# Kernel tuning notes

Hardware: AMD Instinct MI355X
Metric: run time of the kernel (lower is better)

## Reference

```python
import jax, jax.numpy as jnp
import numpy as np

GROUPS = 32
EPS = 1e-5
NUM_HEADS = 8

def group_norm(x, w, b):
    # x: [B, C, H, W], normalize over (C//G, H, W) per group
    B, C, H, W = x.shape
    xg = x.reshape(B, GROUPS, C // GROUPS, H, W)
    mean = xg.mean(axis=(2, 3, 4), keepdims=True)
    var = xg.var(axis=(2, 3, 4), keepdims=True)
    xg = (xg - mean) * jax.lax.rsqrt(var + EPS)
    x = xg.reshape(B, C, H, W)
    return x * w[None, :, None, None] + b[None, :, None, None]

def setup_inputs() -> dict:
    key = jax.random.key(0)
    ks = jax.random.split(key, 3)
    C = 512
    x = jax.random.normal(ks[0], (8, C, 32, 32), dtype=jnp.float32)
    gn_w = jnp.ones((C,), jnp.float32)
    gn_b = jnp.zeros((C,), jnp.float32)
    # 1x1 conv weights stored as [out, in] matrices
    qkv_w = jax.random.normal(ks[1], (3 * C, C), dtype=jnp.float32) * (C ** -0.5)
    qkv_b = jnp.zeros((3 * C,), jnp.float32)
    proj_w = jax.random.normal(ks[2], (C, C), dtype=jnp.float32) * (C ** -0.5)
    proj_b = jnp.zeros((C,), jnp.float32)
    return {"x": x, "gn_w": gn_w, "gn_b": gn_b, "qkv_w": qkv_w,
            "qkv_b": qkv_b, "proj_w": proj_w, "proj_b": proj_b}

def reference(x, gn_w, gn_b, qkv_w, qkv_b, proj_w, proj_b):
    B, C, H, W = x.shape
    nh = NUM_HEADS
    hd = C // nh
    N = H * W
    residual = x
    xn = group_norm(x, gn_w, gn_b)
    # 1x1 conv == channel matmul: [B, 3C, H, W]
    qkv = jnp.einsum('bchw,oc->bohw', xn, qkv_w) + qkv_b[None, :, None, None]
    # [B, 3, nh, hd, N] -> q/k/v each [B, nh, N, hd]
    qkv = qkv.reshape(B, 3, nh, hd, N).transpose(1, 0, 2, 4, 3)
    q, k, v = qkv[0], qkv[1], qkv[2]
    scale = hd ** -0.5
    attn = jnp.einsum('bhqd,bhkd->bhqk', q, k) * scale
    attn = jax.nn.softmax(attn, axis=-1)
    out = jnp.einsum('bhqk,bhkd->bhqd', attn, v)  # [B, nh, N, hd]
    out = out.transpose(0, 1, 3, 2).reshape(B, C, H, W)
    out = jnp.einsum('bchw,oc->bohw', out, proj_w) + proj_b[None, :, None, None]
    return out + residual
```

## Files before the change

kernel.cpp:

```cpp
#include <hip/hip_runtime.h>


typedef __bf16 bf16;
typedef __bf16 bf16x8 __attribute__((ext_vector_type(8)));
typedef __bf16 bf16x4 __attribute__((ext_vector_type(4)));
typedef float  f32x4  __attribute__((ext_vector_type(4)));
typedef float  f32x16 __attribute__((ext_vector_type(16)));
typedef unsigned u32x4 __attribute__((ext_vector_type(4)));

#define MFMA_16x16x32(A, B, C) __builtin_amdgcn_mfma_f32_16x16x32_bf16((A), (B), (C), 0, 0, 0)
#define MFMA_32x32x16(A, B, C) __builtin_amdgcn_mfma_f32_32x32x16_bf16((A), (B), (C), 0, 0, 0)

static __device__ __forceinline__ unsigned cvt_pk_bf16(float a, float b) {
  unsigned r;
  asm("v_cvt_pk_bf16_f32 %0, %1, %2" : "=v"(r) : "v"(a), "v"(b));
  return r;
}

static __device__ __forceinline__ void async_stage_128x32(
    const bf16* __restrict__ g0, bf16* lds, int tid) {
  const int wv = tid >> 6, ln = tid & 63;
#pragma unroll
  for (int cc = 0; cc < 2; ++cc) {
    const int c = wv + cc * 4;
    const bf16* g = g0 + (size_t)(c * 16 + (ln >> 2)) * 512 + (ln & 3) * 8;
    __builtin_amdgcn_global_load_lds(
        (const __attribute__((address_space(1))) void*)g,
        (__attribute__((address_space(3))) void*)(lds + c * 512),
        16, 0, 0);
  }
}

static __device__ __forceinline__ void async_stage_64x32(
    const bf16* __restrict__ g0, bf16* lds, int tid) {
  const int wv = tid >> 6, ln = tid & 63;
  const bf16* g = g0 + (size_t)(wv * 16 + (ln >> 2)) * 512 + (ln & 3) * 8;
  __builtin_amdgcn_global_load_lds(
      (const __attribute__((address_space(1))) void*)g,
      (__attribute__((address_space(3))) void*)(lds + wv * 512),
      16, 0, 0);
}

__global__ __launch_bounds__(256) void gn_fused_kernel(
    const float* __restrict__ x,
    const float* __restrict__ gn_w, const float* __restrict__ gn_b,
    const float* __restrict__ qw, const float* __restrict__ pw,
    bf16* __restrict__ wq, bf16* __restrict__ wp, bf16* __restrict__ xn_t) {
  const int t = threadIdx.x;
  if (blockIdx.x >= 256) {
    const int idx = (blockIdx.x - 256) * 256 + t;
    if (idx < 196608) {
      float4 v = ((const float4*)qw)[idx];
      bf16x4 o = { (bf16)v.x, (bf16)v.y, (bf16)v.z, (bf16)v.w };
      *(bf16x4*)(&wq[idx * 4]) = o;
    }
    if (idx < 65536) {
      float4 v = ((const float4*)pw)[idx];
      bf16x4 o = { (bf16)v.x, (bf16)v.y, (bf16)v.z, (bf16)v.w };
      *(bf16x4*)(&wp[idx * 4]) = o;
    }
    return;
  }
  const int bg = blockIdx.x;
  const int b = bg >> 5, g = bg & 31;
  const int c0 = g * 16;
  const float4* p = (const float4*)(x + ((size_t)b * 512 + c0) * 1024);
  float4 v[16];
  float s = 0.f, s2 = 0.f;
#pragma unroll
  for (int i = 0; i < 16; ++i) {
    v[i] = p[t + 256 * i];
    s  += (v[i].x + v[i].y) + (v[i].z + v[i].w);
    s2 += (v[i].x * v[i].x + v[i].y * v[i].y) + (v[i].z * v[i].z + v[i].w * v[i].w);
  }
#pragma unroll
  for (int d = 1; d < 64; d <<= 1) {
    s  += __shfl_xor(s,  d);
    s2 += __shfl_xor(s2, d);
  }
  __shared__ float as[4], as2[4];
  __shared__ float scs[16], shs[16];
  if ((t & 63) == 0) { as[t >> 6] = s; as2[t >> 6] = s2; }
  __syncthreads();
  if (t < 16) {
    float S  = as[0] + as[1] + as[2] + as[3];
    float S2 = as2[0] + as2[1] + as2[2] + as2[3];
    float m  = S * (1.0f / 16384.0f);
    float rs = rsqrtf(S2 * (1.0f / 16384.0f) - m * m + 1e-5f);
    float sc = rs * gn_w[c0 + t];
    scs[t] = sc;
    shs[t] = gn_b[c0 + t] - m * sc;
  }
  __syncthreads();
  bf16* ob = xn_t + ((size_t)b * 1024 + 4 * t) * 512 + c0;
#pragma unroll
  for (int j = 0; j < 4; ++j) {
    bf16 tmp[16];
#pragma unroll
    for (int i = 0; i < 16; ++i) {
      float val = (j == 0) ? v[i].x : (j == 1) ? v[i].y : (j == 2) ? v[i].z : v[i].w;
      tmp[i] = (bf16)(val * scs[i] + shs[i]);
    }
    *(bf16x8*)(ob + (size_t)j * 512)     = *(bf16x8*)(tmp);
    *(bf16x8*)(ob + (size_t)j * 512 + 8) = *(bf16x8*)(tmp + 8);
  }
}

__global__ __launch_bounds__(256) void qkv_gemm_kernel(
    const bf16* __restrict__ W, const bf16* __restrict__ xn_t,
    const float* __restrict__ qkv_b, bf16* __restrict__ qkv_t,
    bf16* __restrict__ v_t) {
  const int n0 = blockIdx.x * 128;
  const int o0 = blockIdx.y * 128;
  const int b  = blockIdx.z;
  __shared__ bf16 As[2][128 * 32];
  __shared__ bf16 Bs[2][128 * 32];
  const int tid = threadIdx.x, ln = tid & 63, wv = tid >> 6;
  const int mw = (wv >> 1) * 64, nw = (wv & 1) * 64;
  const int l15 = ln & 15, lg = ln >> 4;
  const bool isV = (o0 >= 1024);
  const bf16* gA = W + (size_t)o0 * 512;
  const bf16* gB = xn_t + ((size_t)b * 1024 + n0) * 512;
  f32x4 acc[4][4] = {};
  async_stage_128x32(gA, As[0], tid);
  async_stage_128x32(gB, Bs[0], tid);
  for (int it = 0; it < 16; ++it) {
    __syncthreads();
    const int cur = it & 1, nxt = cur ^ 1;
    if (it < 15) {
      async_stage_128x32(gA + (it + 1) * 32, As[nxt], tid);
      async_stage_128x32(gB + (it + 1) * 32, Bs[nxt], tid);
    }
    bf16x8 af[4], bfr[4];
#pragma unroll
    for (int mi = 0; mi < 4; ++mi)
      af[mi] = *(const bf16x8*)(&As[cur][(mw + mi * 16 + l15) * 32 + lg * 8]);
#pragma unroll
    for (int nj = 0; nj < 4; ++nj)
      bfr[nj] = *(const bf16x8*)(&Bs[cur][(nw + nj * 16 + l15) * 32 + lg * 8]);
    if (!isV) {
#pragma unroll
      for (int mi = 0; mi < 4; ++mi)
#pragma unroll
        for (int nj = 0; nj < 4; ++nj)
          acc[mi][nj] = MFMA_16x16x32(af[mi], bfr[nj], acc[mi][nj]);
    } else {
#pragma unroll
      for (int mi = 0; mi < 4; ++mi)
#pragma unroll
        for (int nj = 0; nj < 4; ++nj)
          acc[mi][nj] = MFMA_16x16x32(bfr[nj], af[mi], acc[mi][nj]);
    }
  }
  if (!isV) {
    const float qs = (o0 < 512) ? 0.125f * 1.44269504089f : 1.0f;
#pragma unroll
    for (int mi = 0; mi < 4; ++mi) {
      const int o = o0 + mw + mi * 16 + lg * 4;
      const float b0 = qkv_b[o], b1 = qkv_b[o + 1], b2 = qkv_b[o + 2], b3 = qkv_b[o + 3];
#pragma unroll
      for (int nj = 0; nj < 4; ++nj) {
        const int n = n0 + nw + nj * 16 + l15;
        f32x4 v = acc[mi][nj];
        bf16x4 st = { (bf16)((v.x + b0) * qs), (bf16)((v.y + b1) * qs),
                      (bf16)((v.z + b2) * qs), (bf16)((v.w + b3) * qs) };
        *(bf16x4*)(&qkv_t[((size_t)b * 1024 + n) * 1536 + o]) = st;
      }
    }
  } else {
#pragma unroll
    for (int mi = 0; mi < 4; ++mi) {
      const int o  = o0 + mw + mi * 16 + l15;
      const int hd = o - 1024;
      const float bias = qkv_b[o];
#pragma unroll
      for (int nj = 0; nj < 4; ++nj) {
        const int n = n0 + nw + nj * 16 + lg * 4;
        f32x4 v = acc[mi][nj];
        bf16x4 st = { (bf16)(v.x + bias), (bf16)(v.y + bias),
                      (bf16)(v.z + bias), (bf16)(v.w + bias) };
        *(bf16x4*)(&v_t[((size_t)b * 512 + hd) * 1024 + n]) = st;
      }
    }
  }
}

__global__ __launch_bounds__(512, 4) void attn_kernel(
    const bf16* __restrict__ qkv_t, const bf16* __restrict__ v_t,
    bf16* __restrict__ at_t) {
  const int qt = blockIdx.y;
  const int b  = blockIdx.x >> 3;
  const int h  = blockIdx.x & 7;
  __shared__ __align__(16) char smem[73728];
  const int tid = threadIdx.x, ln = tid & 63, wv = tid >> 6;
  const int half = wv >> 2, w4 = wv & 3;
  const int l31 = ln & 31, hi = ln >> 5;
  const bf16* hq  = qkv_t + (size_t)b * 1024 * 1536 + h * 64;
  const bf16* hk  = hq + 512;
  const bf16* vtb = v_t + (size_t)(b * 8 + h) * 64 * 1024;

  const int qb = qt * 128 + w4 * 32;
  bf16x8 qf[4];
#pragma unroll
  for (int ks = 0; ks < 4; ++ks)
    qf[ks] = *(const bf16x8*)(hq + (size_t)(qb + l31) * 1536 + ks * 16 + hi * 8);

  f32x16 oacc[2] = {};
  float lst = 0.f;

  const int t256 = tid & 255;
  const int srow = t256 >> 2, scg = (t256 & 3) * 16;
  const int kt0 = half * 8;

  bf16x8 k0r, k1r, v0r, v1r;
  {
    const bf16* gk = hk  + (size_t)(kt0 * 64 + srow) * 1536 + scg;
    const bf16* gv = vtb + (size_t)srow * 1024 + kt0 * 64 + scg;
    k0r = *(const bf16x8*)(gk);
    k1r = *(const bf16x8*)(gk + 8);
    v0r = *(const bf16x8*)(gv);
    v1r = *(const bf16x8*)(gv + 8);
    bf16* Kt = (bf16*)(smem + half * 18432);
    bf16* Vt = Kt + 64 * 72;
    *(bf16x8*)(&Kt[srow * 72 + scg])     = k0r;
    *(bf16x8*)(&Kt[srow * 72 + scg + 8]) = k1r;
    *(bf16x8*)(&Vt[srow * 72 + scg])     = v0r;
    *(bf16x8*)(&Vt[srow * 72 + scg + 8]) = v1r;
  }

  for (int i = 0; i < 8; ++i) {
    __syncthreads();
    if (i < 7) {
      const int kt = kt0 + i + 1;
      const bf16* gk = hk  + (size_t)(kt * 64 + srow) * 1536 + scg;
      const bf16* gv = vtb + (size_t)srow * 1024 + kt * 64 + scg;
      k0r = *(const bf16x8*)(gk);
      k1r = *(const bf16x8*)(gk + 8);
      v0r = *(const bf16x8*)(gv);
      v1r = *(const bf16x8*)(gv + 8);
    }
    const bf16* Kt = (const bf16*)(smem + (i & 1) * 36864 + half * 18432);
    const bf16* Vt = Kt + 64 * 72;

#pragma unroll
    for (int kk = 0; kk < 2; ++kk) {
      const int kvb = kk * 32;
      f32x16 st = {};
      __builtin_amdgcn_s_setprio(1);
#pragma unroll
      for (int ks = 0; ks < 4; ++ks) {
        bf16x8 kf = *(const bf16x8*)(&Kt[(kvb + l31) * 72 + ks * 16 + hi * 8]);
        st = MFMA_32x32x16(kf, qf[ks], st);
      }
      __builtin_amdgcn_s_setprio(0);
#pragma unroll
      for (int r = 0; r < 16; ++r) st[r] = exp2f(st[r]);
      lst += ((st[0] + st[1]) + (st[2] + st[3])) + ((st[4] + st[5]) + (st[6] + st[7]))
           + ((st[8] + st[9]) + (st[10] + st[11])) + ((st[12] + st[13]) + (st[14] + st[15]));
#pragma unroll
      for (int t = 0; t < 2; ++t) {
        unsigned x0 = cvt_pk_bf16(st[t * 8 + 0], st[t * 8 + 1]);
        unsigned x1 = cvt_pk_bf16(st[t * 8 + 2], st[t * 8 + 3]);
        unsigned y0 = cvt_pk_bf16(st[t * 8 + 4], st[t * 8 + 5]);
        unsigned y1 = cvt_pk_bf16(st[t * 8 + 6], st[t * 8 + 7]);
        asm("v_permlane32_swap_b32 %0, %1" : "+v"(x0), "+v"(y0));
        asm("v_permlane32_swap_b32 %0, %1" : "+v"(x1), "+v"(y1));
        u32x4 pu = { x0, x1, y0, y1 };
        bf16x8 pb = __builtin_bit_cast(bf16x8, pu);
        __builtin_amdgcn_s_setprio(1);
#pragma unroll
        for (int dt = 0; dt < 2; ++dt) {
          bf16x8 vf = *(const bf16x8*)(&Vt[(dt * 32 + l31) * 72 + kvb + t * 16 + hi * 8]);
          oacc[dt] = MFMA_32x32x16(vf, pb, oacc[dt]);
        }
        __builtin_amdgcn_s_setprio(0);
      }
    }

    if (i < 7) {
      bf16* Ktn = (bf16*)(smem + ((i + 1) & 1) * 36864 + half * 18432);
      bf16* Vtn = Ktn + 64 * 72;
      *(bf16x8*)(&Ktn[srow * 72 + scg])     = k0r;
      *(bf16x8*)(&Ktn[srow * 72 + scg + 8]) = k1r;
      *(bf16x8*)(&Vtn[srow * 72 + scg])     = v0r;
      *(bf16x8*)(&Vtn[srow * 72 + scg + 8]) = v1r;
    }
  }

  const float lf = lst + __shfl_xor(lst, 32);

  float* MB  = (float*)smem;
  float* MLb = (float*)(smem + 34816);
  __syncthreads();
  if (half == 1) {
    float* mb = MB + w4 * (32 * 68);
#pragma unroll
    for (int dt = 0; dt < 2; ++dt)
#pragma unroll
      for (int rr = 0; rr < 4; ++rr) {
        f32x4 v = { oacc[dt][rr * 4 + 0], oacc[dt][rr * 4 + 1],
                    oacc[dt][rr * 4 + 2], oacc[dt][rr * 4 + 3] };
        *(f32x4*)(mb + l31 * 68 + dt * 32 + rr * 8 + hi * 4) = v;
      }
    if (hi == 0) MLb[w4 * 32 + l31] = lf;
  }
  __syncthreads();
  if (half == 0) {
    const float* mb = MB + w4 * (32 * 68);
    const float inv = 1.0f / (lf + MLb[w4 * 32 + l31]);
    const int q = qb + l31;
    bf16* ob = at_t + ((size_t)b * 1024 + q) * 512 + h * 64;
#pragma unroll
    for (int dt = 0; dt < 2; ++dt)
#pragma unroll
      for (int rr = 0; rr < 4; ++rr) {
        f32x4 obv = *(const f32x4*)(mb + l31 * 68 + dt * 32 + rr * 8 + hi * 4);
        bf16x4 ov = { (bf16)((oacc[dt][rr * 4 + 0] + obv[0]) * inv),
                      (bf16)((oacc[dt][rr * 4 + 1] + obv[1]) * inv),
                      (bf16)((oacc[dt][rr * 4 + 2] + obv[2]) * inv),
                      (bf16)((oacc[dt][rr * 4 + 3] + obv[3]) * inv) };
        *(bf16x4*)(ob + dt * 32 + rr * 8 + hi * 4) = ov;
      }
  }
}

__global__ __launch_bounds__(256) void proj_gemm_kernel(
    const bf16* __restrict__ at_t, const bf16* __restrict__ wp,
    const float* __restrict__ proj_b, const float* __restrict__ x,
    float* __restrict__ out) {
  const int i0 = blockIdx.x * 64;
  const int c0 = blockIdx.y * 128;
  const int b  = blockIdx.z;
  __shared__ bf16 As[2][64 * 32];
  __shared__ bf16 Bs[2][128 * 32];
  const int tid = threadIdx.x, ln = tid & 63, wv = tid >> 6;
  const int mw = (wv >> 1) * 32, nw = (wv & 1) * 64;
  const int l15 = ln & 15, lg = ln >> 4;
  const bf16* gA = at_t + ((size_t)b * 1024 + i0) * 512;
  const bf16* gB = wp + (size_t)c0 * 512;
  f32x4 acc[2][4] = {};
  async_stage_64x32(gA, As[0], tid);
  async_stage_128x32(gB, Bs[0], tid);
  for (int it = 0; it < 16; ++it) {
    __syncthreads();
    const int cur = it & 1, nxt = cur ^ 1;
    if (it < 15) {
      async_stage_64x32(gA + (it + 1) * 32, As[nxt], tid);
      async_stage_128x32(gB + (it + 1) * 32, Bs[nxt], tid);
    }
    bf16x8 af[2], bfr[4];
#pragma unroll
    for (int mi = 0; mi < 2; ++mi)
      af[mi] = *(const bf16x8*)(&As[cur][(mw + mi * 16 + l15) * 32 + lg * 8]);
#pragma unroll
    for (int nj = 0; nj < 4; ++nj)
      bfr[nj] = *(const bf16x8*)(&Bs[cur][(nw + nj * 16 + l15) * 32 + lg * 8]);
#pragma unroll
    for (int mi = 0; mi < 2; ++mi)
#pragma unroll
      for (int nj = 0; nj < 4; ++nj)
        acc[mi][nj] = MFMA_16x16x32(af[mi], bfr[nj], acc[mi][nj]);
  }
#pragma unroll
  for (int mi = 0; mi < 2; ++mi) {
    const int i = i0 + mw + mi * 16 + lg * 4;
#pragma unroll
    for (int nj = 0; nj < 4; ++nj) {
      const int c = c0 + nw + nj * 16 + l15;
      const float bias = proj_b[c];
      const size_t off = ((size_t)b * 512 + c) * 1024 + i;
      const float4 res = *(const float4*)(x + off);
      f32x4 v = acc[mi][nj];
      float4 ov;
      ov.x = v.x + bias + res.x;
      ov.y = v.y + bias + res.y;
      ov.z = v.z + bias + res.z;
      ov.w = v.w + bias + res.w;
      *(float4*)(out + off) = ov;
    }
  }
}

extern "C" void kernel_launch(void* const* d_in, const int* in_sizes, int n_in,
                              void* d_out, int out_size, void* d_ws, size_t ws_size,
                              hipStream_t stream) {
  (void)in_sizes; (void)n_in; (void)out_size; (void)ws_size;
  const float* x      = (const float*)d_in[0];
  const float* gn_w   = (const float*)d_in[1];
  const float* gn_b   = (const float*)d_in[2];
  const float* qkv_w  = (const float*)d_in[3];
  const float* qkv_b  = (const float*)d_in[4];
  const float* proj_w = (const float*)d_in[5];
  const float* proj_b = (const float*)d_in[6];
  float* out = (float*)d_out;

  char* ws = (char*)d_ws;
  bf16* wq    = (bf16*)ws;
  bf16* wp    = wq + (size_t)1536 * 512;
  bf16* xn_t  = wp + (size_t)512 * 512;
  bf16* qkv_t = xn_t + (size_t)8 * 1024 * 512;
  bf16* at_t  = qkv_t + (size_t)8 * 1024 * 1536;
  bf16* v_t   = at_t + (size_t)8 * 1024 * 512;

  hipLaunchKernelGGL(gn_fused_kernel, dim3(1280),     dim3(256), 0, stream,
                     x, gn_w, gn_b, qkv_w, proj_w, wq, wp, xn_t);
  hipLaunchKernelGGL(qkv_gemm_kernel, dim3(8, 12, 8), dim3(256), 0, stream,
                     wq, xn_t, qkv_b, qkv_t, v_t);
  hipLaunchKernelGGL(attn_kernel,     dim3(64, 8),    dim3(512), 0, stream,
                     qkv_t, v_t, at_t);
  hipLaunchKernelGGL(proj_gemm_kernel,dim3(16, 4, 8), dim3(256), 0, stream,
                     at_t, wp, proj_b, x, out);
}
```

Baseline: 156.7 us.

## Stage attention K/V tiles via async global_load_lds with XOR-swizzled LDS

```diff
diff --git a/kernel.cpp b/kernel.cpp
--- a/kernel.cpp
+++ b/kernel.cpp
@@ -185,13 +185,38 @@
   }
 }
 
+static __device__ __forceinline__ void attn_stage(
+    const bf16* __restrict__ hk, const bf16* __restrict__ vtb,
+    char* bufbase, int it, int wv, int ln) {
+  const int hh = wv >> 2;
+  const int kt = hh * 8 + it;
+  const int r8 = ln >> 3;
+  const int e0 = ((ln & 7) ^ r8) * 8;
+  char* base = bufbase + hh * 16384;
+#pragma unroll
+  for (int j = 0; j < 2; ++j) {
+    const int g = (wv & 3) * 2 + j;
+    const int row = g * 8 + r8;
+    const bf16* gk = hk + (size_t)(kt * 64 + row) * 1536 + e0;
+    __builtin_amdgcn_global_load_lds(
+        (const __attribute__((address_space(1))) void*)gk,
+        (__attribute__((address_space(3))) void*)(base + g * 1024),
+        16, 0, 0);
+    const bf16* gv = vtb + (size_t)row * 1024 + kt * 64 + e0;
+    __builtin_amdgcn_global_load_lds(
+        (const __attribute__((address_space(1))) void*)gv,
+        (__attribute__((address_space(3))) void*)(base + 8192 + g * 1024),
+        16, 0, 0);
+  }
+}
+
 __global__ __launch_bounds__(512, 4) void attn_kernel(
     const bf16* __restrict__ qkv_t, const bf16* __restrict__ v_t,
     bf16* __restrict__ at_t) {
   const int qt = blockIdx.y;
   const int b  = blockIdx.x >> 3;
   const int h  = blockIdx.x & 7;
-  __shared__ __align__(16) char smem[73728];
+  __shared__ __align__(16) char smem[65536];
   const int tid = threadIdx.x, ln = tid & 63, wv = tid >> 6;
   const int half = wv >> 2, w4 = wv & 3;
   const int l31 = ln & 31, hi = ln >> 5;
@@ -208,51 +233,26 @@
   f32x16 oacc[2] = {};
   float lst = 0.f;
 
-  const int t256 = tid & 255;
-  const int srow = t256 >> 2, scg = (t256 & 3) * 16;
-  const int kt0 = half * 8;
-
-  bf16x8 k0r, k1r, v0r, v1r;
-  {
-    const bf16* gk = hk  + (size_t)(kt0 * 64 + srow) * 1536 + scg;
-    const bf16* gv = vtb + (size_t)srow * 1024 + kt0 * 64 + scg;
-    k0r = *(const bf16x8*)(gk);
-    k1r = *(const bf16x8*)(gk + 8);
-    v0r = *(const bf16x8*)(gv);
-    v1r = *(const bf16x8*)(gv + 8);
-    bf16* Kt = (bf16*)(smem + half * 18432);
-    bf16* Vt = Kt + 64 * 72;
-    *(bf16x8*)(&Kt[srow * 72 + scg])     = k0r;
-    *(bf16x8*)(&Kt[srow * 72 + scg + 8]) = k1r;
-    *(bf16x8*)(&Vt[srow * 72 + scg])     = v0r;
-    *(bf16x8*)(&Vt[srow * 72 + scg + 8]) = v1r;
-  }
+  attn_stage(hk, vtb, smem, 0, wv, ln);
 
   for (int i = 0; i < 8; ++i) {
     __syncthreads();
-    if (i < 7) {
-      const int kt = kt0 + i + 1;
-      const bf16* gk = hk  + (size_t)(kt * 64 + srow) * 1536 + scg;
-      const bf16* gv = vtb + (size_t)srow * 1024 + kt * 64 + scg;
-      k0r = *(const bf16x8*)(gk);
-      k1r = *(const bf16x8*)(gk + 8);
-      v0r = *(const bf16x8*)(gv);
-      v1r = *(const bf16x8*)(gv + 8);
-    }
-    const bf16* Kt = (const bf16*)(smem + (i & 1) * 36864 + half * 18432);
-    const bf16* Vt = Kt + 64 * 72;
+    if (i < 7)
+      attn_stage(hk, vtb, smem + ((i + 1) & 1) * 32768, i + 1, wv, ln);
+    const bf16* Kt = (const bf16*)(smem + (i & 1) * 32768 + half * 16384);
+    const bf16* Vt = Kt + 64 * 64;
 
 #pragma unroll
     for (int kk = 0; kk < 2; ++kk) {
       const int kvb = kk * 32;
+      const int krow = kvb + l31;
+      const int ksw = (krow & 7) * 8;
       f32x16 st = {};
-      __builtin_amdgcn_s_setprio(1);
 #pragma unroll
       for (int ks = 0; ks < 4; ++ks) {
-        bf16x8 kf = *(const bf16x8*)(&Kt[(kvb + l31) * 72 + ks * 16 + hi * 8]);
+        bf16x8 kf = *(const bf16x8*)(&Kt[krow * 64 + ((ks * 16 + hi * 8) ^ ksw)]);
         st = MFMA_32x32x16(kf, qf[ks], st);
       }
-      __builtin_amdgcn_s_setprio(0);
 #pragma unroll
       for (int r = 0; r < 16; ++r) st[r] = exp2f(st[r]);
       lst += ((st[0] + st[1]) + (st[2] + st[3])) + ((st[4] + st[5]) + (st[6] + st[7]))
@@ -267,23 +267,14 @@
         asm("v_permlane32_swap_b32 %0, %1" : "+v"(x1), "+v"(y1));
         u32x4 pu = { x0, x1, y0, y1 };
         bf16x8 pb = __builtin_bit_cast(bf16x8, pu);
-        __builtin_amdgcn_s_setprio(1);
 #pragma unroll
         for (int dt = 0; dt < 2; ++dt) {
-          bf16x8 vf = *(const bf16x8*)(&Vt[(dt * 32 + l31) * 72 + kvb + t * 16 + hi * 8]);
+          const int vrow = dt * 32 + l31;
+          bf16x8 vf = *(const bf16x8*)(
+              &Vt[vrow * 64 + ((kvb + t * 16 + hi * 8) ^ ((vrow & 7) * 8))]);
           oacc[dt] = MFMA_32x32x16(vf, pb, oacc[dt]);
         }
-        __builtin_amdgcn_s_setprio(0);
-      }
-    }
-
-    if (i < 7) {
-      bf16* Ktn = (bf16*)(smem + ((i + 1) & 1) * 36864 + half * 18432);
-      bf16* Vtn = Ktn + 64 * 72;
-      *(bf16x8*)(&Ktn[srow * 72 + scg])     = k0r;
-      *(bf16x8*)(&Ktn[srow * 72 + scg + 8]) = k1r;
-      *(bf16x8*)(&Vtn[srow * 72 + scg])     = v0r;
-      *(bf16x8*)(&Vtn[srow * 72 + scg + 8]) = v1r;
+      }
     }
   }
 
```

Result: no change. 154.9 us (-1.1%).
